# Kernel tuning notes

Measured on AMD Instinct MI355X. Metric: run time of the kernel, lower is better.

The kernel has to match this reference:

```python
import jax, jax.numpy as jnp
import numpy as np

BN_EPS = 1e-5


def setup_inputs() -> dict:
    key = jax.random.key(0)
    ks = jax.random.split(key, 10)
    B, C, N = 16, 512, 4096
    Cr = C // 4
    s = 0.05
    return {
        "x": jax.random.normal(ks[0], (B, C, N), dtype=jnp.float32),
        # channel attention MLP (1x1 convs on pooled vector)
        "w1": jax.random.normal(ks[1], (Cr, C), dtype=jnp.float32) * s,
        "b1": jnp.zeros((Cr,), jnp.float32),
        "w2": jax.random.normal(ks[2], (C, Cr), dtype=jnp.float32) * s,
        "b2": jnp.zeros((C,), jnp.float32),
        # spatial attention branch
        "w3": jax.random.normal(ks[3], (Cr, C), dtype=jnp.float32) * s,
        "b3": jnp.zeros((Cr,), jnp.float32),
        "bn_gamma": jnp.ones((Cr,), jnp.float32),
        "bn_beta": jnp.zeros((Cr,), jnp.float32),
        "bn_mean": jnp.zeros((Cr,), jnp.float32),
        "bn_var": jnp.ones((Cr,), jnp.float32),
        "w4": jax.random.normal(ks[4], (1, Cr), dtype=jnp.float32) * s,
        "b4": jnp.zeros((1,), jnp.float32),
    }


def reference(x, w1, b1, w2, b2, w3, b3, bn_gamma, bn_beta, bn_mean, bn_var, w4, b4):
    # x: [B, C, N]; inference semantics (Dropout = identity, BN uses running stats)
    # ---- channel attention ----
    pooled = jnp.mean(x, axis=-1)                        # [B, C] (AdaptiveAvgPool1d(1))
    h = jax.nn.relu(pooled @ w1.T + b1)                  # [B, C/4]
    ca = jax.nn.sigmoid(h @ w2.T + b2)[:, :, None]       # [B, C, 1]
    x_ca = x * ca                                        # [B, C, N]
    # ---- spatial attention ----
    h2 = jnp.einsum('oc,bcn->bon', w3, x_ca) + b3[:, None]    # [B, C/4, N]
    inv = bn_gamma / jnp.sqrt(bn_var + BN_EPS)                 # [C/4]
    h2 = h2 * inv[:, None] + (bn_beta - bn_mean * inv)[:, None]
    h2 = jax.nn.relu(h2)
    sa = jax.nn.sigmoid(jnp.einsum('oc,bcn->bon', w4, h2) + b4[:, None])  # [B, 1, N]
    return x + x_ca * sa
```

## Files before the change

### kernel.cpp

```cpp
#include <hip/hip_runtime.h>
#include <math.h>

constexpr int B  = 16;
constexpr int C  = 512;
constexpr int N  = 4096;
constexpr int CR = 128;
constexpr int NT = 128;
constexpr int KC = 64;

typedef __attribute__((ext_vector_type(8))) short bf16x8;
typedef __attribute__((ext_vector_type(4))) float f32x4;

__device__ __forceinline__ float sigmoidf_(float v) {
    return 1.0f / (1.0f + __expf(-v));
}
__device__ __forceinline__ unsigned f2bf(float f) {
    unsigned u = __float_as_uint(f);
    u += 0x7fffu + ((u >> 16) & 1u);
    return u >> 16;
}

#define LGKM_BARRIER() do {                                   \
    asm volatile("s_waitcnt lgkmcnt(0)" ::: "memory");        \
    __builtin_amdgcn_s_barrier();                             \
    asm volatile("" ::: "memory");                            \
} while (0)

__global__ __launch_bounds__(256) void k_pre(
    const float* __restrict__ x, float* __restrict__ pooled,
    const float* __restrict__ w3, const float* __restrict__ b3,
    const float* __restrict__ gamma, const float* __restrict__ beta,
    const float* __restrict__ mean, const float* __restrict__ var,
    unsigned short* __restrict__ w3f, float* __restrict__ bias2)
{
    if (blockIdx.x < 2048) {
        int w    = threadIdx.x >> 6;
        int lane = threadIdx.x & 63;
        int row  = blockIdx.x * 4 + w;
        const float4* xr = (const float4*)(x + (size_t)row * N);
        float s = 0.f;
        #pragma unroll
        for (int i = 0; i < 16; ++i) {
            float4 v = xr[i * 64 + lane];
            s += v.x + v.y + v.z + v.w;
        }
        #pragma unroll
        for (int off = 32; off; off >>= 1) s += __shfl_xor(s, off, 64);
        if (lane == 0) pooled[row] = s * (1.0f / N);
    } else {
        int idx  = (blockIdx.x - 2048) * 256 + threadIdx.x;
        int g    = idx >> 6;
        int lane = idx & 63;
        int ck   = g >> 4;
        int kk   = (g >> 3) & 1;
        int ob   = g & 7;
        int o    = ob * 16 + (lane & 15);
        int c    = ck * 64 + kk * 32 + (lane >> 4) * 8;
        float inv = gamma[o] * rsqrtf(var[o] + 1e-5f);
        float4 a  = *(const float4*)(w3 + o * C + c);
        float4 bq = *(const float4*)(w3 + o * C + c + 4);
        unsigned r0 = f2bf(a.x * inv)  | (f2bf(a.y * inv) << 16);
        unsigned r1 = f2bf(a.z * inv)  | (f2bf(a.w * inv) << 16);
        unsigned r2 = f2bf(bq.x * inv) | (f2bf(bq.y * inv) << 16);
        unsigned r3 = f2bf(bq.z * inv) | (f2bf(bq.w * inv) << 16);
        *(uint4*)((char*)w3f + (size_t)idx * 16) = make_uint4(r0, r1, r2, r3);
        if (idx < CR) {
            float iv = gamma[idx] * rsqrtf(var[idx] + 1e-5f);
            bias2[idx] = b3[idx] * iv + beta[idx] - mean[idx] * iv;
        }
    }
}

__global__ __launch_bounds__(256) void k_ca(
    const float* __restrict__ pooled,
    const float* __restrict__ w1, const float* __restrict__ b1,
    const float* __restrict__ w2, const float* __restrict__ b2,
    const unsigned short* __restrict__ w3f,
    float* __restrict__ ca, unsigned short* __restrict__ w3b)
{
    __shared__ float ps[C];
    __shared__ float hs[CR];
    __shared__ float ca_s[C];
    int b = blockIdx.x, t = threadIdx.x;
    ps[t] = pooled[b * C + t];
    ps[t + 256] = pooled[b * C + t + 256];
    __syncthreads();

    if (t < CR) {
        float acc = b1[t];
        const float4* wr = (const float4*)(w1 + t * C);
        const float4* pr = (const float4*)ps;
        #pragma unroll 4
        for (int i = 0; i < C / 4; ++i) {
            float4 wv = wr[i], pv = pr[i];
            acc += wv.x * pv.x + wv.y * pv.y + wv.z * pv.z + wv.w * pv.w;
        }
        hs[t] = fmaxf(acc, 0.f);
    }
    __syncthreads();

    #pragma unroll
    for (int k = 0; k < 2; ++k) {
        int c2 = t + k * 256;
        float a = b2[c2];
        const float4* w2r = (const float4*)(w2 + c2 * CR);
        const float4* hr  = (const float4*)hs;
        #pragma unroll 4
        for (int i = 0; i < CR / 4; ++i) {
            float4 wv = w2r[i], hv = hr[i];
            a += wv.x * hv.x + wv.y * hv.y + wv.z * hv.z + wv.w * hv.w;
        }
        float cav = sigmoidf_(a);
        ca_s[c2] = cav;
        ca[b * C + c2] = cav;
    }
    __syncthreads();

    #pragma unroll 4
    for (int j = 0; j < 32; ++j) {
        int i    = j * 256 + t;
        int g    = i >> 6;
        int lane = i & 63;
        int ck   = g >> 4;
        int kk   = (g >> 3) & 1;
        int c0   = ck * 64 + kk * 32 + ((lane >> 4) << 3);
        uint4 wv = *(const uint4*)((const char*)w3f + (size_t)i * 16);
        const float* cb = &ca_s[c0];
        uint4 ov;
        {
            float lo = __uint_as_float(wv.x << 16), hi = __uint_as_float(wv.x & 0xffff0000u);
            ov.x = f2bf(lo * cb[0]) | (f2bf(hi * cb[1]) << 16);
        }
        {
            float lo = __uint_as_float(wv.y << 16), hi = __uint_as_float(wv.y & 0xffff0000u);
            ov.y = f2bf(lo * cb[2]) | (f2bf(hi * cb[3]) << 16);
        }
        {
            float lo = __uint_as_float(wv.z << 16), hi = __uint_as_float(wv.z & 0xffff0000u);
            ov.z = f2bf(lo * cb[4]) | (f2bf(hi * cb[5]) << 16);
        }
        {
            float lo = __uint_as_float(wv.w << 16), hi = __uint_as_float(wv.w & 0xffff0000u);
            ov.w = f2bf(lo * cb[6]) | (f2bf(hi * cb[7]) << 16);
        }
        *(uint4*)((char*)w3b + ((size_t)b * 8192 + i) * 16) = ov;
    }
}

__global__ __launch_bounds__(512, 2) void k_gemm(
    const float* __restrict__ x, const unsigned short* __restrict__ w3b,
    const float* __restrict__ bias2, const float* __restrict__ w4,
    const float* __restrict__ b4, float* __restrict__ sa)
{
    __shared__ __align__(16) short lds_x[2][NT * KC];
    __shared__ float red[4][NT];
    __shared__ float bias2_s[CR];
    __shared__ float w4_s[CR];

    const int t    = threadIdx.x;
    const int lane = t & 63;
    const int w    = t >> 6;
    const int b    = blockIdx.y;
    const int n0   = blockIdx.x * NT;
    const int wo   = (w & 3) * 32;
    const int wn   = (w >> 2) * 64;
    const int ob0  = (w & 3) * 2;

    const size_t xbase = (size_t)b * C * N + n0;
    const int ng = t & 63;
    const int cg = t >> 6;

    if (t < CR) { bias2_s[t] = bias2[t]; w4_s[t] = w4[t]; }

    float2 xva[8], xvb[8];

#define LOADX(dst, CK) do { const int c0_ = (CK) * KC;                         \
    _Pragma("unroll") for (int ci = 0; ci < 8; ++ci)                           \
        dst[ci] = *(const float2*)(x + xbase + (size_t)(c0_ + cg * 8 + ci) * N + 2 * ng); \
} while (0)

#define CONVERT_WRITE(src, BUF) do {                                           \
    unsigned q0[4], q1[4];                                                     \
    _Pragma("unroll") for (int h = 0; h < 4; ++h) {                            \
        q0[h] = f2bf(src[2 * h].x) | (f2bf(src[2 * h + 1].x) << 16);           \
        q1[h] = f2bf(src[2 * h].y) | (f2bf(src[2 * h + 1].y) << 16);           \
    }                                                                          \
    int nl0 = 2 * ng, nl1 = 2 * ng + 1;                                        \
    int a0 = (nl0 * 128 + cg * 16) ^ ((nl0 & 7) << 4);                         \
    int a1 = (nl1 * 128 + cg * 16) ^ ((nl1 & 7) << 4);                         \
    *(uint4*)((char*)lds_x[BUF] + a0) = make_uint4(q0[0], q0[1], q0[2], q0[3]);\
    *(uint4*)((char*)lds_x[BUF] + a1) = make_uint4(q1[0], q1[1], q1[2], q1[3]);\
} while (0)

    LOADX(xva, 0);
    LOADX(xvb, 1);
    CONVERT_WRITE(xva, 0);

    f32x4 acc[2][4];
    #pragma unroll
    for (int i = 0; i < 2; ++i)
        #pragma unroll
        for (int j = 0; j < 4; ++j) acc[i][j] = (f32x4)0.f;

    const char* wb = (const char*)w3b + (size_t)b * 131072;

    #pragma unroll
    for (int ck = 0; ck < 8; ++ck) {
        if (ck < 6) { if (ck & 1) LOADX(xvb, ck + 2); else LOADX(xva, ck + 2); }

        LGKM_BARRIER();

        #pragma unroll
        for (int kk = 0; kk < 2; ++kk) {
            bf16x8 af[2];
            #pragma unroll
            for (int i = 0; i < 2; ++i) {
                int g = ck * 16 + kk * 8 + ob0 + i;
                af[i] = *(const bf16x8*)(wb + (size_t)(g * 64 + lane) * 16);
            }
            bf16x8 bfr[4];
            #pragma unroll
            for (int j = 0; j < 4; ++j) {
                int br = wn + j * 16 + (lane & 15);
                int bb = (br * 128 + kk * 64 + (lane >> 4) * 16) ^ ((br & 7) << 4);
                bfr[j] = *(const bf16x8*)((const char*)lds_x[ck & 1] + bb);
            }
            #pragma unroll
            for (int i = 0; i < 2; ++i)
                #pragma unroll
                for (int j = 0; j < 4; ++j)
                    acc[i][j] = __builtin_amdgcn_mfma_f32_16x16x32_bf16(af[i], bfr[j], acc[i][j], 0, 0, 0);
        }
        if (ck < 7) { if (ck & 1) CONVERT_WRITE(xva, 0); else CONVERT_WRITE(xvb, 1); }
    }

    #pragma unroll
    for (int j = 0; j < 4; ++j) {
        float p = 0.f;
        #pragma unroll
        for (int i = 0; i < 2; ++i) {
            #pragma unroll
            for (int r = 0; r < 4; ++r) {
                int o = wo + i * 16 + ((lane >> 4) << 2) + r;
                p = fmaf(w4_s[o], fmaxf(acc[i][j][r] + bias2_s[o], 0.f), p);
            }
        }
        p += __shfl_xor(p, 16, 64);
        p += __shfl_xor(p, 32, 64);
        if (lane < 16) red[w & 3][wn + j * 16 + lane] = p;
    }
    __syncthreads();
    if (t < NT)
        sa[b * N + n0 + t] = sigmoidf_(red[0][t] + red[1][t] + red[2][t] + red[3][t] + b4[0]);
#undef LOADX
#undef CONVERT_WRITE
}

__global__ __launch_bounds__(256) void k_out(
    const float* __restrict__ x, const float* __restrict__ ca,
    const float* __restrict__ sa, float* __restrict__ out)
{
    const float4* x4  = (const float4*)x;
    const float4* sa4 = (const float4*)sa;
    float4* o4        = (float4*)out;
    int base = blockIdx.x * 256 + threadIdx.x;
    #pragma unroll 4
    for (int it = 0; it < 16; ++it) {
        int i4 = base + it * 524288;
        float4 v  = x4[i4];
        int b  = i4 >> 19;
        int c  = (i4 >> 10) & 511;
        int n4 = i4 & 1023;
        float cav = ca[b * 512 + c];
        float4 sv = sa4[b * 1024 + n4];
        float4 r;
        r.x = v.x * fmaf(cav, sv.x, 1.0f);
        r.y = v.y * fmaf(cav, sv.y, 1.0f);
        r.z = v.z * fmaf(cav, sv.z, 1.0f);
        r.w = v.w * fmaf(cav, sv.w, 1.0f);
        o4[i4] = r;
    }
}

extern "C" void kernel_launch(void* const* d_in, const int* in_sizes, int n_in,
                              void* d_out, int out_size, void* d_ws, size_t ws_size,
                              hipStream_t stream)
{
    const float* x   = (const float*)d_in[0];
    const float* w1  = (const float*)d_in[1];
    const float* b1  = (const float*)d_in[2];
    const float* w2  = (const float*)d_in[3];
    const float* b2  = (const float*)d_in[4];
    const float* w3  = (const float*)d_in[5];
    const float* b3  = (const float*)d_in[6];
    const float* g   = (const float*)d_in[7];
    const float* be  = (const float*)d_in[8];
    const float* mn  = (const float*)d_in[9];
    const float* vr  = (const float*)d_in[10];
    const float* w4  = (const float*)d_in[11];
    const float* b4  = (const float*)d_in[12];
    float* out = (float*)d_out;

    float* ws     = (float*)d_ws;
    float* pooled = ws;
    float* ca     = ws + 8192;
    float* bias2  = ws + 16384;
    unsigned short* w3f = (unsigned short*)(ws + 16640);
    unsigned short* w3b = (unsigned short*)(ws + 49408);
    float* sa     = ws + 573696;

    k_pre<<<2048 + 32, 256, 0, stream>>>(x, pooled, w3, b3, g, be, mn, vr, w3f, bias2);
    k_ca<<<B, 256, 0, stream>>>(pooled, w1, b1, w2, b2, w3f, ca, w3b);
    dim3 g3(N / NT, B);
    k_gemm<<<g3, 512, 0, stream>>>(x, w3b, bias2, w4, b4, sa);
    k_out<<<2048, 256, 0, stream>>>(x, ca, sa, out);
}
```

Measured before the change: 124.9 us.

## Materialize a bf16 copy of x in the pooling pass and reuse it downstream

```diff
diff --git a/kernel.cpp b/kernel.cpp
--- a/kernel.cpp
+++ b/kernel.cpp
@@ -10,6 +10,8 @@
 
 typedef __attribute__((ext_vector_type(8))) short bf16x8;
 typedef __attribute__((ext_vector_type(4))) float f32x4;
+typedef __attribute__((ext_vector_type(4))) unsigned short u16x4;
+typedef __attribute__((ext_vector_type(8))) unsigned short u16x8;
 
 __device__ __forceinline__ float sigmoidf_(float v) {
     return 1.0f / (1.0f + __expf(-v));
@@ -18,6 +20,9 @@
     unsigned u = __float_as_uint(f);
     u += 0x7fffu + ((u >> 16) & 1u);
     return u >> 16;
+}
+__device__ __forceinline__ float bf2f(unsigned short s) {
+    return __uint_as_float((unsigned)s << 16);
 }
 
 #define LGKM_BARRIER() do {                                   \
@@ -31,18 +36,28 @@
     const float* __restrict__ w3, const float* __restrict__ b3,
     const float* __restrict__ gamma, const float* __restrict__ beta,
     const float* __restrict__ mean, const float* __restrict__ var,
-    unsigned short* __restrict__ w3f, float* __restrict__ bias2)
+    unsigned short* __restrict__ w3f, float* __restrict__ bias2,
+    unsigned short* __restrict__ xb, int do_xb)
 {
     if (blockIdx.x < 2048) {
         int w    = threadIdx.x >> 6;
         int lane = threadIdx.x & 63;
         int row  = blockIdx.x * 4 + w;
         const float4* xr = (const float4*)(x + (size_t)row * N);
+        unsigned short* xbr = xb + (size_t)row * N;
         float s = 0.f;
         #pragma unroll
         for (int i = 0; i < 16; ++i) {
             float4 v = xr[i * 64 + lane];
             s += v.x + v.y + v.z + v.w;
+            if (do_xb) {
+                u16x4 o;
+                o[0] = (unsigned short)f2bf(v.x);
+                o[1] = (unsigned short)f2bf(v.y);
+                o[2] = (unsigned short)f2bf(v.z);
+                o[3] = (unsigned short)f2bf(v.w);
+                *(u16x4*)(xbr + 4 * (i * 64 + lane)) = o;
+            }
         }
         #pragma unroll
         for (int off = 32; off; off >>= 1) s += __shfl_xor(s, off, 64);
@@ -147,8 +162,8 @@
     }
 }
 
-__global__ __launch_bounds__(512, 2) void k_gemm(
-    const float* __restrict__ x, const unsigned short* __restrict__ w3b,
+__global__ __launch_bounds__(512, 2) void k_gemm_b16(
+    const unsigned short* __restrict__ xb, const unsigned short* __restrict__ w3b,
     const float* __restrict__ bias2, const float* __restrict__ w4,
     const float* __restrict__ b4, float* __restrict__ sa)
 {
@@ -166,6 +181,143 @@
     const int wn   = (w >> 2) * 64;
     const int ob0  = (w & 3) * 2;
 
+    const int q = t & 31;
+    const int g = t >> 5;
+    const size_t xrow = (size_t)b * C * N + n0;
+
+    if (t < CR) { bias2_s[t] = bias2[t]; w4_s[t] = w4[t]; }
+
+    u16x4 xva[4], xvb[4];
+
+#define LOADX(dst, CK) do { const int c0_ = (CK) * KC;                         \
+    _Pragma("unroll") for (int ci = 0; ci < 4; ++ci)                           \
+        dst[ci] = *(const u16x4*)(xb + xrow + (size_t)(c0_ + 4 * g + ci) * N + 4 * q); \
+} while (0)
+
+#define CONVERT_WRITE(src, BUF) do {                                           \
+    _Pragma("unroll") for (int j = 0; j < 4; ++j) {                            \
+        unsigned u0 = (unsigned)src[0][j] | ((unsigned)src[1][j] << 16);       \
+        unsigned u1 = (unsigned)src[2][j] | ((unsigned)src[3][j] << 16);       \
+        int n_ = 4 * q + j;                                                    \
+        int byte = (n_ * 128 + g * 8) ^ ((n_ & 7) << 4);                       \
+        *(uint2*)((char*)lds_x[BUF] + byte) = make_uint2(u0, u1);              \
+    }                                                                          \
+} while (0)
+
+    LOADX(xva, 0);
+    LOADX(xvb, 1);
+    CONVERT_WRITE(xva, 0);
+
+    f32x4 acc[2][4];
+    #pragma unroll
+    for (int i = 0; i < 2; ++i)
+        #pragma unroll
+        for (int j = 0; j < 4; ++j) acc[i][j] = (f32x4)0.f;
+
+    const char* wb = (const char*)w3b + (size_t)b * 131072;
+
+    #pragma unroll
+    for (int ck = 0; ck < 8; ++ck) {
+        if (ck < 6) { if (ck & 1) LOADX(xvb, ck + 2); else LOADX(xva, ck + 2); }
+
+        LGKM_BARRIER();
+
+        #pragma unroll
+        for (int kk = 0; kk < 2; ++kk) {
+            bf16x8 af[2];
+            #pragma unroll
+            for (int i = 0; i < 2; ++i) {
+                int gg = ck * 16 + kk * 8 + ob0 + i;
+                af[i] = *(const bf16x8*)(wb + (size_t)(gg * 64 + lane) * 16);
+            }
+            bf16x8 bfr[4];
+            #pragma unroll
+            for (int j = 0; j < 4; ++j) {
+                int br = wn + j * 16 + (lane & 15);
+                int bb = (br * 128 + kk * 64 + (lane >> 4) * 16) ^ ((br & 7) << 4);
+                bfr[j] = *(const bf16x8*)((const char*)lds_x[ck & 1] + bb);
+            }
+            #pragma unroll
+            for (int i = 0; i < 2; ++i)
+                #pragma unroll
+                for (int j = 0; j < 4; ++j)
+                    acc[i][j] = __builtin_amdgcn_mfma_f32_16x16x32_bf16(af[i], bfr[j], acc[i][j], 0, 0, 0);
+        }
+        if (ck < 7) { if (ck & 1) CONVERT_WRITE(xva, 0); else CONVERT_WRITE(xvb, 1); }
+    }
+
+    #pragma unroll
+    for (int j = 0; j < 4; ++j) {
+        float p = 0.f;
+        #pragma unroll
+        for (int i = 0; i < 2; ++i) {
+            #pragma unroll
+            for (int r = 0; r < 4; ++r) {
+                int o = wo + i * 16 + ((lane >> 4) << 2) + r;
+                p = fmaf(w4_s[o], fmaxf(acc[i][j][r] + bias2_s[o], 0.f), p);
+            }
+        }
+        p += __shfl_xor(p, 16, 64);
+        p += __shfl_xor(p, 32, 64);
+        if (lane < 16) red[w & 3][wn + j * 16 + lane] = p;
+    }
+    __syncthreads();
+    if (t < NT)
+        sa[b * N + n0 + t] = sigmoidf_(red[0][t] + red[1][t] + red[2][t] + red[3][t] + b4[0]);
+#undef LOADX
+#undef CONVERT_WRITE
+}
+
+__global__ __launch_bounds__(256) void k_out_b16(
+    const unsigned short* __restrict__ xb, const float* __restrict__ ca,
+    const float* __restrict__ sa, float* __restrict__ out)
+{
+    const float4* sa4 = (const float4*)sa;
+    float4* o4        = (float4*)out;
+    int base = blockIdx.x * 256 + threadIdx.x;
+    #pragma unroll 2
+    for (int it = 0; it < 8; ++it) {
+        size_t i8 = (size_t)base + (size_t)it * 524288;
+        u16x8 v = *(const u16x8*)(xb + i8 * 8);
+        int b  = (int)(i8 >> 18);
+        int c  = (int)(i8 >> 9) & 511;
+        int n8 = (int)i8 & 511;
+        float cav = ca[b * 512 + c];
+        float4 s0 = sa4[b * 1024 + n8 * 2];
+        float4 s1 = sa4[b * 1024 + n8 * 2 + 1];
+        float4 r0, r1;
+        r0.x = bf2f(v[0]) * fmaf(cav, s0.x, 1.0f);
+        r0.y = bf2f(v[1]) * fmaf(cav, s0.y, 1.0f);
+        r0.z = bf2f(v[2]) * fmaf(cav, s0.z, 1.0f);
+        r0.w = bf2f(v[3]) * fmaf(cav, s0.w, 1.0f);
+        r1.x = bf2f(v[4]) * fmaf(cav, s1.x, 1.0f);
+        r1.y = bf2f(v[5]) * fmaf(cav, s1.y, 1.0f);
+        r1.z = bf2f(v[6]) * fmaf(cav, s1.z, 1.0f);
+        r1.w = bf2f(v[7]) * fmaf(cav, s1.w, 1.0f);
+        o4[i8 * 2]     = r0;
+        o4[i8 * 2 + 1] = r1;
+    }
+}
+
+__global__ __launch_bounds__(512, 2) void k_gemm_f32(
+    const float* __restrict__ x, const unsigned short* __restrict__ w3b,
+    const float* __restrict__ bias2, const float* __restrict__ w4,
+    const float* __restrict__ b4, float* __restrict__ sa)
+{
+    __shared__ __align__(16) short lds_x[2][NT * KC];
+    __shared__ float red[4][NT];
+    __shared__ float bias2_s[CR];
+    __shared__ float w4_s[CR];
+
+    const int t    = threadIdx.x;
+    const int lane = t & 63;
+    const int w    = t >> 6;
+    const int b    = blockIdx.y;
+    const int n0   = blockIdx.x * NT;
+    const int wo   = (w & 3) * 32;
+    const int wn   = (w >> 2) * 64;
+    const int ob0  = (w & 3) * 2;
+
     const size_t xbase = (size_t)b * C * N + n0;
     const int ng = t & 63;
     const int cg = t >> 6;
@@ -178,7 +330,6 @@
     _Pragma("unroll") for (int ci = 0; ci < 8; ++ci)                           \
         dst[ci] = *(const float2*)(x + xbase + (size_t)(c0_ + cg * 8 + ci) * N + 2 * ng); \
 } while (0)
-
 #define CONVERT_WRITE(src, BUF) do {                                           \
     unsigned q0[4], q1[4];                                                     \
     _Pragma("unroll") for (int h = 0; h < 4; ++h) {                            \
@@ -207,16 +358,14 @@
     #pragma unroll
     for (int ck = 0; ck < 8; ++ck) {
         if (ck < 6) { if (ck & 1) LOADX(xvb, ck + 2); else LOADX(xva, ck + 2); }
-
         LGKM_BARRIER();
-
         #pragma unroll
         for (int kk = 0; kk < 2; ++kk) {
             bf16x8 af[2];
             #pragma unroll
             for (int i = 0; i < 2; ++i) {
-                int g = ck * 16 + kk * 8 + ob0 + i;
-                af[i] = *(const bf16x8*)(wb + (size_t)(g * 64 + lane) * 16);
+                int gg = ck * 16 + kk * 8 + ob0 + i;
+                af[i] = *(const bf16x8*)(wb + (size_t)(gg * 64 + lane) * 16);
             }
             bf16x8 bfr[4];
             #pragma unroll
@@ -233,6 +382,8 @@
         }
         if (ck < 7) { if (ck & 1) CONVERT_WRITE(xva, 0); else CONVERT_WRITE(xvb, 1); }
     }
+#undef LOADX
+#undef CONVERT_WRITE
 
     #pragma unroll
     for (int j = 0; j < 4; ++j) {
@@ -252,11 +403,9 @@
     __syncthreads();
     if (t < NT)
         sa[b * N + n0 + t] = sigmoidf_(red[0][t] + red[1][t] + red[2][t] + red[3][t] + b4[0]);
-#undef LOADX
-#undef CONVERT_WRITE
-}
-
-__global__ __launch_bounds__(256) void k_out(
+}
+
+__global__ __launch_bounds__(256) void k_out_f32(
     const float* __restrict__ x, const float* __restrict__ ca,
     const float* __restrict__ sa, float* __restrict__ out)
 {
@@ -308,10 +457,20 @@
     unsigned short* w3f = (unsigned short*)(ws + 16640);
     unsigned short* w3b = (unsigned short*)(ws + 49408);
     float* sa     = ws + 573696;
-
-    k_pre<<<2048 + 32, 256, 0, stream>>>(x, pooled, w3, b3, g, be, mn, vr, w3f, bias2);
+    unsigned short* xb = (unsigned short*)(ws + 639232);
+
+    const size_t need = (size_t)639232 * 4 + (size_t)B * C * N * 2;
+    const int use_xb = (ws_size >= need) ? 1 : 0;
+
+    k_pre<<<2048 + 32, 256, 0, stream>>>(x, pooled, w3, b3, g, be, mn, vr,
+                                         w3f, bias2, xb, use_xb);
     k_ca<<<B, 256, 0, stream>>>(pooled, w1, b1, w2, b2, w3f, ca, w3b);
     dim3 g3(N / NT, B);
-    k_gemm<<<g3, 512, 0, stream>>>(x, w3b, bias2, w4, b4, sa);
-    k_out<<<2048, 256, 0, stream>>>(x, ca, sa, out);
-}
+    if (use_xb) {
+        k_gemm_b16<<<g3, 512, 0, stream>>>(xb, w3b, bias2, w4, b4, sa);
+        k_out_b16<<<2048, 256, 0, stream>>>(xb, ca, sa, out);
+    } else {
+        k_gemm_f32<<<g3, 512, 0, stream>>>(x, w3b, bias2, w4, b4, sa);
+        k_out_f32<<<2048, 256, 0, stream>>>(x, ca, sa, out);
+    }
+}
```

Result: slower. 132.7 us (+6.2%).

## Fuse spatial-attention GEMM and output scaling into one kernel with wider tiles

Applied to the files above, without the earlier changes.

```diff
diff --git a/kernel.cpp b/kernel.cpp
--- a/kernel.cpp
+++ b/kernel.cpp
@@ -5,7 +5,7 @@
 constexpr int C  = 512;
 constexpr int N  = 4096;
 constexpr int CR = 128;
-constexpr int NT = 128;
+constexpr int NT = 256;
 constexpr int KC = 64;
 
 typedef __attribute__((ext_vector_type(8))) short bf16x8;
@@ -147,12 +147,15 @@
     }
 }
 
-__global__ __launch_bounds__(512, 2) void k_gemm(
-    const float* __restrict__ x, const unsigned short* __restrict__ w3b,
-    const float* __restrict__ bias2, const float* __restrict__ w4,
-    const float* __restrict__ b4, float* __restrict__ sa)
+__global__ __launch_bounds__(1024, 1) void k_main(
+    const float* __restrict__ x, const float* __restrict__ ca,
+    const unsigned short* __restrict__ w3b, const float* __restrict__ bias2,
+    const float* __restrict__ w4, const float* __restrict__ b4,
+    float* __restrict__ out)
 {
     __shared__ __align__(16) short lds_x[2][NT * KC];
+    __shared__ float ca_s[C];
+    __shared__ __align__(16) float sa_s[NT];
     __shared__ float red[4][NT];
     __shared__ float bias2_s[CR];
     __shared__ float w4_s[CR];
@@ -167,10 +170,11 @@
     const int ob0  = (w & 3) * 2;
 
     const size_t xbase = (size_t)b * C * N + n0;
-    const int ng = t & 63;
-    const int cg = t >> 6;
-
-    if (t < CR) { bias2_s[t] = bias2[t]; w4_s[t] = w4[t]; }
+    const int ng = t & 127;
+    const int cg = t >> 7;
+
+    if (t < 512) ca_s[t] = ca[b * C + t];
+    if (t < CR)  { bias2_s[t] = bias2[t]; w4_s[t] = w4[t]; }
 
     float2 xva[8], xvb[8];
 
@@ -215,8 +219,8 @@
             bf16x8 af[2];
             #pragma unroll
             for (int i = 0; i < 2; ++i) {
-                int g = ck * 16 + kk * 8 + ob0 + i;
-                af[i] = *(const bf16x8*)(wb + (size_t)(g * 64 + lane) * 16);
+                int gg = ck * 16 + kk * 8 + ob0 + i;
+                af[i] = *(const bf16x8*)(wb + (size_t)(gg * 64 + lane) * 16);
             }
             bf16x8 bfr[4];
             #pragma unroll
@@ -251,35 +255,27 @@
     }
     __syncthreads();
     if (t < NT)
-        sa[b * N + n0 + t] = sigmoidf_(red[0][t] + red[1][t] + red[2][t] + red[3][t] + b4[0]);
+        sa_s[t] = sigmoidf_(red[0][t] + red[1][t] + red[2][t] + red[3][t] + b4[0]);
+    __syncthreads();
+
+    #pragma unroll 4
+    for (int it = 0; it < 32; ++it) {
+        int f4 = it * 1024 + t;
+        int c  = f4 >> 6;
+        int n4 = f4 & 63;
+        size_t off = xbase + (size_t)c * N + n4 * 4;
+        float4 v = *(const float4*)(x + off);
+        float cav = ca_s[c];
+        float4 sv = *(const float4*)&sa_s[n4 * 4];
+        float4 o4;
+        o4.x = v.x * fmaf(cav, sv.x, 1.0f);
+        o4.y = v.y * fmaf(cav, sv.y, 1.0f);
+        o4.z = v.z * fmaf(cav, sv.z, 1.0f);
+        o4.w = v.w * fmaf(cav, sv.w, 1.0f);
+        *(float4*)(out + off) = o4;
+    }
 #undef LOADX
 #undef CONVERT_WRITE
-}
-
-__global__ __launch_bounds__(256) void k_out(
-    const float* __restrict__ x, const float* __restrict__ ca,
-    const float* __restrict__ sa, float* __restrict__ out)
-{
-    const float4* x4  = (const float4*)x;
-    const float4* sa4 = (const float4*)sa;
-    float4* o4        = (float4*)out;
-    int base = blockIdx.x * 256 + threadIdx.x;
-    #pragma unroll 4
-    for (int it = 0; it < 16; ++it) {
-        int i4 = base + it * 524288;
-        float4 v  = x4[i4];
-        int b  = i4 >> 19;
-        int c  = (i4 >> 10) & 511;
-        int n4 = i4 & 1023;
-        float cav = ca[b * 512 + c];
-        float4 sv = sa4[b * 1024 + n4];
-        float4 r;
-        r.x = v.x * fmaf(cav, sv.x, 1.0f);
-        r.y = v.y * fmaf(cav, sv.y, 1.0f);
-        r.z = v.z * fmaf(cav, sv.z, 1.0f);
-        r.w = v.w * fmaf(cav, sv.w, 1.0f);
-        o4[i4] = r;
-    }
 }
 
 extern "C" void kernel_launch(void* const* d_in, const int* in_sizes, int n_in,
@@ -307,11 +303,9 @@
     float* bias2  = ws + 16384;
     unsigned short* w3f = (unsigned short*)(ws + 16640);
     unsigned short* w3b = (unsigned short*)(ws + 49408);
-    float* sa     = ws + 573696;
 
     k_pre<<<2048 + 32, 256, 0, stream>>>(x, pooled, w3, b3, g, be, mn, vr, w3f, bias2);
     k_ca<<<B, 256, 0, stream>>>(pooled, w1, b1, w2, b2, w3f, ca, w3b);
     dim3 g3(N / NT, B);
-    k_gemm<<<g3, 512, 0, stream>>>(x, w3b, bias2, w4, b4, sa);
-    k_out<<<2048, 256, 0, stream>>>(x, ca, sa, out);
-}
+    k_main<<<g3, 1024, 0, stream>>>(x, ca, w3b, bias2, w4, b4, out);
+}
```

After: 135.9 us. 8.9% more time.
